# Kernel tuning notes

Hardware: AMD Instinct MI355X
Metric: run time of the kernel (lower is better)

The kernel has to match this reference:

```python
import jax, jax.numpy as jnp
import numpy as np

K_NEIGHBORS = 16
N_CLASSES = 10


def setup_inputs() -> dict:
    key = jax.random.key(0)
    k1, k2, k3 = jax.random.split(key, 3)
    x = jax.random.normal(k1, (2048, 128), dtype=jnp.float32)
    train_data = jax.random.normal(k2, (100000, 128), dtype=jnp.float32)
    train_labels = jax.random.randint(k3, (100000,), 0, N_CLASSES, dtype=jnp.int64)
    return {"x": x, "train_data": train_data, "train_labels": train_labels}


def reference(x, train_data, train_labels):
    N = x.shape[0]
    x2 = jnp.sum(x * x, axis=1, keepdims=True)            # [N, 1]
    t2 = jnp.sum(train_data * train_data, axis=1)          # [M]
    d2 = x2 + t2[None, :] - 2.0 * (x @ train_data.T)       # [N, M]
    dist = jnp.sqrt(jnp.maximum(d2, 0.0))
    # smallest-k via top_k on negated distances
    neg_d, idx = jax.lax.top_k(-dist, K_NEIGHBORS)         # [N, K]
    d = -neg_d
    labels = train_labels[idx]                              # [N, K]
    # weights == 'distance': inverse distance; rows containing an exact match
    # (inf weight) get a 0/1 indicator vector instead.
    w = 1.0 / d
    inf_mask = jnp.isinf(w)
    inf_row = jnp.any(inf_mask, axis=1, keepdims=True)
    w = jnp.where(inf_row, inf_mask.astype(jnp.float32), w)
    # weighted vote: scatter-add weights into per-class buckets
    rows = jnp.arange(N)[:, None]
    proba = jnp.zeros((N, N_CLASSES), jnp.float32).at[rows, labels].add(w)
    s = jnp.sum(proba, axis=1, keepdims=True)
    s = jnp.where(s == 0.0, 1.0, s)
    proba = proba / s
    pred = jnp.argmax(proba, axis=1)
    return pred, proba
```

## Files before the change

kernel.cpp:

```cpp
#include <hip/hip_runtime.h>
#include <hip/hip_fp16.h>
#include <math.h>

#define M_TRAIN 100000
#define NQ 2048
#define DIM 128
#define KNN 16
#define NCLS 10

#define S_STRIDE 16
#define S_CNT (M_TRAIN / S_STRIDE)
#define S_PAD 6272
#define SCH 49
#define SPC 128
#define TT 64
#define MQ 128
#define QSTR 136

#define CAP 768
#define TBH 50176
#define NTR 128
#define NQT 64
#define MARGIN 3.0f

using bfrag = __attribute__((ext_vector_type(8))) short;
using cfrag = __attribute__((ext_vector_type(4))) float;

__device__ __forceinline__ bool better(float d1, int i1, float d2, int i2) {
    return (d1 < d2) || (d1 == d2 && i1 < i2);
}

__device__ __forceinline__ unsigned pack_bf16(float a, float b) {
    unsigned ua = __float_as_uint(a), ub = __float_as_uint(b);
    ua += 0x7fffu + ((ua >> 16) & 1u);
    ub += 0x7fffu + ((ub >> 16) & 1u);
    return (ua >> 16) | (ub & 0xffff0000u);
}

__device__ __forceinline__ void gload_lds16(const void* g, void* l) {
    __builtin_amdgcn_global_load_lds(
        (const __attribute__((address_space(1))) unsigned int*)g,
        (__attribute__((address_space(3))) unsigned int*)l, 16, 0, 0);
}

__global__ void knn_norms(const float* __restrict__ train,
                          const float* __restrict__ x,
                          float* __restrict__ t2, float* __restrict__ x2) {
    int gw = (blockIdx.x * blockDim.x + threadIdx.x) >> 6;
    int lane = threadIdx.x & 63;
    if (gw >= M_TRAIN + NQ) return;
    const float* r = (gw < M_TRAIN) ? (train + (size_t)gw * DIM)
                                    : (x + (size_t)(gw - M_TRAIN) * DIM);
    float a = r[lane];
    float b = r[lane + 64];
    float s = a * a + b * b;
    #pragma unroll
    for (int off = 32; off > 0; off >>= 1)
        s += __shfl_down(s, off, 64);
    if (lane == 0) {
        if (gw < M_TRAIN) t2[gw] = s; else x2[gw - M_TRAIN] = s;
    }
}

__global__ void knn_zero_cnt(int* __restrict__ cnt) {
    int i = blockIdx.x * blockDim.x + threadIdx.x;
    if (i < NQ) cnt[i] = 0;
}

__global__ __launch_bounds__(256, 2)
void knn_sub_mfma(const float* __restrict__ x, const float* __restrict__ train,
                  const float* __restrict__ t2, const float* __restrict__ x2,
                  __half* __restrict__ dsub) {
    __shared__ short Q[MQ * QSTR];
    __shared__ short T[TT * QSTR];
    __shared__ float t2h[TT];
    int tid = threadIdx.x;
    int w = tid >> 6, lane = tid & 63;
    int rquad = lane >> 4, rcol = lane & 15;
    int qBase = blockIdx.y * MQ;
    int cBase = blockIdx.x * SPC;

    #pragma unroll
    for (int it = 0; it < 16; ++it) {
        int f = it * 256 + tid;
        int row = f >> 5, c4 = f & 31;
        float4 v = ((const float4*)x)[(size_t)(qBase + row) * (DIM / 4) + c4];
        uint2 p; p.x = pack_bf16(v.x, v.y); p.y = pack_bf16(v.z, v.w);
        *(uint2*)&Q[row * QSTR + c4 * 4] = p;
    }
    __syncthreads();

    float x2r[2][4];
    #pragma unroll
    for (int rt = 0; rt < 2; ++rt)
        #pragma unroll
        for (int reg = 0; reg < 4; ++reg)
            x2r[rt][reg] = x2[qBase + w * 32 + rt * 16 + rquad * 4 + reg];

    bfrag A[2][4];
    #pragma unroll
    for (int rt = 0; rt < 2; ++rt)
        #pragma unroll
        for (int ks = 0; ks < 4; ++ks) {
            int r = w * 32 + rt * 16 + rcol;
            A[rt][ks] = *(const bfrag*)&Q[r * QSTR + ks * 32 + rquad * 8];
        }

    const cfrag zero4 = {0.f, 0.f, 0.f, 0.f};
    for (int t = 0; t < 2; ++t) {
        __syncthreads();
        int sBase = cBase + t * TT;
        #pragma unroll
        for (int it = 0; it < 8; ++it) {
            int f = it * 256 + tid;
            int row = f >> 5, c4 = f & 31;
            int sj = sBase + row;
            bool ok = sj < S_CNT;
            float4 v = ok ? ((const float4*)train)[(size_t)sj * S_STRIDE * (DIM / 4) + c4]
                          : make_float4(0.f, 0.f, 0.f, 0.f);
            uint2 p; p.x = pack_bf16(v.x, v.y); p.y = pack_bf16(v.z, v.w);
            *(uint2*)&T[row * QSTR + c4 * 4] = p;
        }
        if (tid < TT) {
            int sj = sBase + tid;
            t2h[tid] = (sj < S_CNT) ? t2[(size_t)sj * S_STRIDE] : 1e30f;
        }
        __syncthreads();

        cfrag acc[2][4];
        #pragma unroll
        for (int ks = 0; ks < 4; ++ks) {
            bfrag B[4];
            #pragma unroll
            for (int ct = 0; ct < 4; ++ct) {
                int n = ct * 16 + rcol;
                B[ct] = *(const bfrag*)&T[n * QSTR + ks * 32 + rquad * 8];
            }
            #pragma unroll
            for (int rt = 0; rt < 2; ++rt)
                #pragma unroll
                for (int ct = 0; ct < 4; ++ct)
                    acc[rt][ct] = (ks == 0)
                        ? __builtin_amdgcn_mfma_f32_16x16x32_bf16(A[rt][0], B[ct], zero4, 0, 0, 0)
                        : __builtin_amdgcn_mfma_f32_16x16x32_bf16(A[rt][ks], B[ct], acc[rt][ct], 0, 0, 0);
        }

        float th[4];
        #pragma unroll
        for (int ct = 0; ct < 4; ++ct) th[ct] = t2h[ct * 16 + rcol];
        #pragma unroll
        for (int rt = 0; rt < 2; ++rt)
            #pragma unroll
            for (int ct = 0; ct < 4; ++ct)
                #pragma unroll
                for (int reg = 0; reg < 4; ++reg) {
                    float d2 = x2r[rt][reg] + th[ct] - 2.f * acc[rt][ct][reg];
                    int qrow = qBase + w * 32 + rt * 16 + rquad * 4 + reg;
                    int col = sBase + ct * 16 + rcol;
                    dsub[(size_t)qrow * S_PAD + col] = __float2half_rn(d2);
                }
    }
}

__global__ __launch_bounds__(256)
void knn_select(const __half* __restrict__ dsub, float* __restrict__ tau) {
    __shared__ float wv[4];
    __shared__ int   wc[4];
    __shared__ float sv;
    __shared__ int   sc;
    int q = blockIdx.x, tid = threadIdx.x;
    int w = tid >> 6, lane = tid & 63;

    float bd[KNN];
    #pragma unroll
    for (int j = 0; j < KNN; ++j) bd[j] = 3.4e38f;
    for (int k = 0; k < 25; ++k) {
        int idx = k * 256 + tid;
        if (idx < S_PAD) {
            float v = __half2float(dsub[(size_t)q * S_PAD + idx]);
            if (v < bd[KNN - 1]) {
                bd[KNN - 1] = v;
                #pragma unroll
                for (int j = KNN - 1; j >= 1; --j)
                    if (bd[j] < bd[j - 1]) { float t = bd[j]; bd[j] = bd[j - 1]; bd[j - 1] = t; }
            }
        }
    }

    float last = 3.4e38f;
    for (int sel = 0; sel < KNN; ++sel) {
        float mv = bd[0]; int mj = 0;
        #pragma unroll
        for (int j = 1; j < KNN; ++j) if (bd[j] < mv) { mv = bd[j]; mj = j; }
        int mc = (tid << 4) | mj;
        #pragma unroll
        for (int off = 32; off > 0; off >>= 1) {
            float ov = __shfl_down(mv, off, 64);
            int   oc = __shfl_down(mc, off, 64);
            if (ov < mv) { mv = ov; mc = oc; }
        }
        if (lane == 0) { wv[w] = mv; wc[w] = mc; }
        __syncthreads();
        if (tid == 0) {
            float bv = wv[0]; int bc = wc[0];
            #pragma unroll
            for (int i = 1; i < 4; ++i) if (wv[i] < bv) { bv = wv[i]; bc = wc[i]; }
            sv = bv; sc = bc;
        }
        __syncthreads();
        last = sv;
        if (tid == (sc >> 4)) {
            int j0 = sc & 15;
            #pragma unroll
            for (int j = 0; j < KNN; ++j) if (j == j0) bd[j] = 3.4e38f;
        }
        __syncthreads();
    }
    if (tid == 0) tau[q] = last;
}

__global__ __launch_bounds__(256)
void knn_convert_bf16(const float* __restrict__ train,
                      unsigned int* __restrict__ tb, int rowBase,
                      const float* __restrict__ x,
                      unsigned int* __restrict__ xb) {
    int b = blockIdx.x;
    if (b >= (TBH * 32) / 256) {
        int i = (b - (TBH * 32) / 256) * 256 + threadIdx.x;
        int row = i >> 5, seg = i & 31;
        float4 v = ((const float4*)x)[(size_t)row * (DIM / 4) + seg];
        uint2 p; p.x = pack_bf16(v.x, v.y); p.y = pack_bf16(v.z, v.w);
        ((uint2*)xb)[(size_t)row * 32 + seg] = p;
        return;
    }
    int i = b * 256 + threadIdx.x;
    int row = i >> 5, seg = i & 31;
    int g = rowBase + row;
    float4 v = (g < M_TRAIN)
        ? ((const float4*)train)[(size_t)g * (DIM / 4) + seg]
        : make_float4(0.f, 0.f, 0.f, 0.f);
    uint2 p; p.x = pack_bf16(v.x, v.y); p.y = pack_bf16(v.z, v.w);
    int off = (seg * 8) ^ ((row & 7) << 4);
    *(uint2*)((char*)tb + (size_t)row * 256 + off) = p;
}

__global__ __launch_bounds__(256, 4)
void knn_filter5(const unsigned int* __restrict__ xbb,
                 const short* __restrict__ tbb,
                 const float* __restrict__ t2, const float* __restrict__ x2,
                 const float* __restrict__ tau, int pBase0,
                 int* __restrict__ buf_i, int* __restrict__ cnt) {
    __shared__ __align__(16) short T[NTR * DIM];
    int tid = threadIdx.x;
    int w = tid >> 6, lane = tid & 63;
    int rquad = lane >> 4, rcol = lane & 15;

    int bid = blockIdx.x;
    int xcd = bid & 7, r = bid >> 3;
    int qb = r & 31;
    int nch = xcd + 8 * (r >> 5);
    int qBase = qb * NQT;
    int tbase = pBase0 + nch * NTR;

    const char* gsrc = (const char*)tbb + (size_t)nch * NTR * 256 + w * 8192 + lane * 16;
    char* ldst = (char*)T + w * 8192;
    #pragma unroll
    for (int i = 0; i < 8; ++i)
        gload_lds16(gsrc + i * 1024, ldst + i * 1024);

    bfrag A[4];
    int qrow = qBase + w * 16 + rcol;
    const char* xrow = (const char*)xbb + (size_t)qrow * 256;
    #pragma unroll
    for (int ks = 0; ks < 4; ++ks)
        A[ks] = *(const bfrag*)(xrow + ks * 64 + rquad * 16);

    float RC[4];
    #pragma unroll
    for (int reg = 0; reg < 4; ++reg) {
        int q = qBase + w * 16 + rquad * 4 + reg;
        RC[reg] = 0.5f * (x2[q] - tau[q] - MARGIN);
    }
    float th[8];
    #pragma unroll
    for (int ct = 0; ct < 8; ++ct)
        th[ct] = 0.5f * t2[tbase + ct * 16 + rcol];
    __syncthreads();

    int swz = (rcol & 7) << 4;
    int cs[4];
    #pragma unroll
    for (int ks = 0; ks < 4; ++ks)
        cs[ks] = (ks * 64 + rquad * 16) ^ swz;

    const cfrag zero4 = {0.f, 0.f, 0.f, 0.f};
    cfrag acc[8];
    #pragma unroll
    for (int ks = 0; ks < 4; ++ks)
        #pragma unroll
        for (int ct = 0; ct < 8; ++ct) {
            const bfrag B = *(const bfrag*)((const char*)T + (ct * 16 + rcol) * 256 + cs[ks]);
            acc[ct] = (ks == 0)
                ? __builtin_amdgcn_mfma_f32_16x16x32_bf16(A[0], B, zero4, 0, 0, 0)
                : __builtin_amdgcn_mfma_f32_16x16x32_bf16(A[ks], B, acc[ct], 0, 0, 0);
        }

    unsigned gm[4][8];
    int tot[4];
    #pragma unroll
    for (int reg = 0; reg < 4; ++reg) {
        int t = 0;
        #pragma unroll
        for (int ct = 0; ct < 8; ++ct) {
            int idx = tbase + ct * 16 + rcol;
            bool pass = (acc[ct][reg] >= RC[reg] + th[ct]) && (idx < M_TRAIN);
            unsigned long long m = __ballot(pass);
            unsigned g = (unsigned)(m >> (rquad * 16)) & 0xFFFFu;
            gm[reg][ct] = g;
            t += __popc(g);
        }
        tot[reg] = t;
    }
    int baseR[4];
    #pragma unroll
    for (int reg = 0; reg < 4; ++reg) {
        int q = qBase + w * 16 + rquad * 4 + reg;
        if (rcol == 0) baseR[reg] = atomicAdd(&cnt[q], tot[reg]);
    }
    int lsrc = lane & 48;
    unsigned lb = 1u << rcol;
    #pragma unroll
    for (int reg = 0; reg < 4; ++reg) {
        int q = qBase + w * 16 + rquad * 4 + reg;
        int b = __shfl(baseR[reg], lsrc, 64);
        int off = 0;
        #pragma unroll
        for (int ct = 0; ct < 8; ++ct) {
            unsigned g = gm[reg][ct];
            if (g & lb) {
                int slot = b + off + __popc(g & (lb - 1));
                if (slot < CAP)
                    buf_i[(size_t)q * CAP + slot] = tbase + ct * 16 + rcol;
            }
            off += __popc(g);
        }
    }
}

__global__ __launch_bounds__(256)
void knn_final(const float* __restrict__ x,
               const float* __restrict__ train,
               const float* __restrict__ t2v,
               const float* __restrict__ x2v,
               const int* __restrict__ buf_i,
               const int* __restrict__ cnt,
               const int* __restrict__ labels,
               float* __restrict__ out) {
    __shared__ float sd[CAP];
    __shared__ int   si[CAP];
    int q = blockIdx.x;
    int tid = threadIdx.x;
    int w = tid >> 6, lane = tid & 63;
    int grp = lane >> 4;
    int sub = lane & 15;
    int n = cnt[q]; if (n > CAP) n = CAP;

    const float4* xq = (const float4*)&x[(size_t)q * DIM + sub * 8];
    float4 qa = xq[0], qb = xq[1];
    float x2l = x2v[q];

    for (int base = 0; base < n; base += 16) {
        int i = base + w * 4 + grp;
        if (i < n) {
            int idx = buf_i[(size_t)q * CAP + i];
            const float4* tr = (const float4*)&train[(size_t)idx * DIM + sub * 8];
            float4 ta = tr[0], tb4 = tr[1];
            float s = qa.x * ta.x + qa.y * ta.y + qa.z * ta.z + qa.w * ta.w
                    + qb.x * tb4.x + qb.y * tb4.y + qb.z * tb4.z + qb.w * tb4.w;
            s += __shfl_xor(s, 1, 64);
            s += __shfl_xor(s, 2, 64);
            s += __shfl_xor(s, 4, 64);
            s += __shfl_xor(s, 8, 64);
            if (sub == 0) { sd[i] = x2l + t2v[idx] - 2.f * s; si[i] = idx; }
        }
    }
    __syncthreads();

    if (w == 0) {
        float bd[12]; int bi2[12];
        #pragma unroll
        for (int j = 0; j < 12; ++j) {
            int i = lane + j * 64;
            if (i < n) { bd[j] = sd[i]; bi2[j] = si[i]; }
            else       { bd[j] = 3.4e38f; bi2[j] = 0x7fffffff; }
        }
        float kd[KNN]; int ki[KNN];
        for (int sel = 0; sel < KNN; ++sel) {
            float md = bd[0]; int mi = bi2[0]; int mc = (lane << 4);
            #pragma unroll
            for (int j = 1; j < 12; ++j)
                if (better(bd[j], bi2[j], md, mi)) { md = bd[j]; mi = bi2[j]; mc = (lane << 4) | j; }
            #pragma unroll
            for (int off = 32; off > 0; off >>= 1) {
                float od = __shfl_down(md, off, 64);
                int   oi = __shfl_down(mi, off, 64);
                int   oc = __shfl_down(mc, off, 64);
                if (better(od, oi, md, mi)) { md = od; mi = oi; mc = oc; }
            }
            md = __shfl(md, 0, 64); mi = __shfl(mi, 0, 64); mc = __shfl(mc, 0, 64);
            kd[sel] = md; ki[sel] = mi;
            if (lane == (mc >> 4)) {
                int j0 = mc & 15;
                #pragma unroll
                for (int j = 0; j < 12; ++j)
                    if (j == j0) { bd[j] = 3.4e38f; bi2[j] = 0x7fffffff; }
            }
        }

        if (lane == 0) {
            bool anyzero = false;
            float dist[KNN];
            #pragma unroll
            for (int j = 0; j < KNN; ++j) {
                dist[j] = sqrtf(fmaxf(kd[j], 0.f));
                if (dist[j] == 0.f) anyzero = true;
            }
            float spr[NCLS];
            #pragma unroll
            for (int c = 0; c < NCLS; ++c) spr[c] = 0.f;
            #pragma unroll
            for (int j = 0; j < KNN; ++j) {
                int idxj = ki[j];
                if (idxj < 0 || idxj >= M_TRAIN) continue;
                float wgt = anyzero ? (dist[j] == 0.f ? 1.f : 0.f) : 1.f / dist[j];
                spr[labels[idxj]] += wgt;
            }
            float s = 0.f;
            #pragma unroll
            for (int c = 0; c < NCLS; ++c) s += spr[c];
            if (s == 0.f) s = 1.f;
            float inv = 1.f / s;
            float best = -1.f; int bc = 0;
            #pragma unroll
            for (int c = 0; c < NCLS; ++c) {
                float pv = spr[c] * inv;
                out[NQ + (size_t)q * NCLS + c] = pv;
                if (pv > best) { best = pv; bc = c; }
            }
            out[q] = (float)bc;
        }
    }
}

extern "C" void kernel_launch(void* const* d_in, const int* in_sizes, int n_in,
                              void* d_out, int out_size, void* d_ws, size_t ws_size,
                              hipStream_t stream) {
    const float* x      = (const float*)d_in[0];
    const float* train  = (const float*)d_in[1];
    const int*   labels = (const int*)d_in[2];
    float* out = (float*)d_out;

    char* base = (char*)d_ws;
    float*  t2   = (float*)(base);
    float*  x2   = (float*)(base + 401408);
    float*  tau  = (float*)(base + 409600);
    int*    cnt  = (int*)  (base + 417792);
    char*   region = base + 425984;
    __half* dsub = (__half*)region;
    unsigned int* tb = (unsigned int*)region;
    int*    bi   = (int*)(region + 12845056);
    unsigned int* xb = (unsigned int*)(region + 19136512);

    int nrows = M_TRAIN + NQ;
    knn_norms<<<(nrows * 64 + 255) / 256, 256, 0, stream>>>(train, x, t2, x2);
    knn_zero_cnt<<<(NQ + 255) / 256, 256, 0, stream>>>(cnt);

    dim3 gs(SCH, NQ / MQ);
    knn_sub_mfma<<<gs, 256, 0, stream>>>(x, train, t2, x2, dsub);

    knn_select<<<NQ, 256, 0, stream>>>(dsub, tau);

    for (int h = 0; h < 2; ++h) {
        int rowBase = h * TBH;
        int cgrid = (TBH * 32) / 256 + (h == 0 ? (NQ * 32) / 256 : 0);
        knn_convert_bf16<<<cgrid, 256, 0, stream>>>(train, tb, rowBase, x, xb);
        knn_filter5<<<(TBH / NTR) * (NQ / NQT), 256, 0, stream>>>(
            xb, (const short*)tb, t2, x2, tau, rowBase, bi, cnt);
    }

    knn_final<<<NQ, 256, 0, stream>>>(x, train, t2, x2, bi, cnt, labels, out);
}
```

Measured before the change: 401.0 us.

## Store approximate bf16 distances in filter and prune candidates before exact rescoring

The filter kernel now also writes an approximate squared distance, taken from its bf16 MFMA accumulator, as fp16 alongside each candidate index. The final kernel selects the 16th smallest approximate distance per query and keeps only candidates within a fixed slack of it. Only those survivors are gathered from the fp32 training rows for exact rescoring. The serial single-wave top-16 selection is replaced by a parallel rank-counting pass. The cost is an extra fp16 buffer write and read, plus a correctness risk if bf16/fp16 error exceeds the slack.

```diff
diff --git a/kernel.cpp b/kernel.cpp
--- a/kernel.cpp
+++ b/kernel.cpp
@@ -22,6 +22,7 @@
 #define NTR 128
 #define NQT 64
 #define MARGIN 3.0f
+#define SLACK 7.0f
 
 using bfrag = __attribute__((ext_vector_type(8))) short;
 using cfrag = __attribute__((ext_vector_type(4))) float;
@@ -245,11 +246,12 @@
 }
 
 __global__ __launch_bounds__(256, 4)
-void knn_filter5(const unsigned int* __restrict__ xbb,
+void knn_filter6(const unsigned int* __restrict__ xbb,
                  const short* __restrict__ tbb,
                  const float* __restrict__ t2, const float* __restrict__ x2,
                  const float* __restrict__ tau, int pBase0,
-                 int* __restrict__ buf_i, int* __restrict__ cnt) {
+                 int* __restrict__ buf_i, __half* __restrict__ buf_h,
+                 int* __restrict__ cnt) {
     __shared__ __align__(16) short T[NTR * DIM];
     int tid = threadIdx.x;
     int w = tid >> 6, lane = tid & 63;
@@ -275,11 +277,12 @@
     for (int ks = 0; ks < 4; ++ks)
         A[ks] = *(const bfrag*)(xrow + ks * 64 + rquad * 16);
 
-    float RC[4];
+    float RC[4], x2q[4];
     #pragma unroll
     for (int reg = 0; reg < 4; ++reg) {
         int q = qBase + w * 16 + rquad * 4 + reg;
-        RC[reg] = 0.5f * (x2[q] - tau[q] - MARGIN);
+        x2q[reg] = x2[q];
+        RC[reg] = 0.5f * (x2q[reg] - tau[q] - MARGIN);
     }
     float th[8];
     #pragma unroll
@@ -339,8 +342,11 @@
             unsigned g = gm[reg][ct];
             if (g & lb) {
                 int slot = b + off + __popc(g & (lb - 1));
-                if (slot < CAP)
+                if (slot < CAP) {
                     buf_i[(size_t)q * CAP + slot] = tbase + ct * 16 + rcol;
+                    float d2a = x2q[reg] + 2.f * th[ct] - 2.f * acc[ct][reg];
+                    buf_h[(size_t)q * CAP + slot] = __float2half_rn(d2a);
+                }
             }
             off += __popc(g);
         }
@@ -353,26 +359,82 @@
                const float* __restrict__ t2v,
                const float* __restrict__ x2v,
                const int* __restrict__ buf_i,
+               const __half* __restrict__ buf_h,
                const int* __restrict__ cnt,
                const int* __restrict__ labels,
                float* __restrict__ out) {
     __shared__ float sd[CAP];
     __shared__ int   si[CAP];
+    __shared__ int   keep[CAP];
+    __shared__ float wk[64];
+    __shared__ int   kr[KNN];
+    __shared__ float sthr;
+    __shared__ int   smcnt;
     int q = blockIdx.x;
     int tid = threadIdx.x;
     int w = tid >> 6, lane = tid & 63;
-    int grp = lane >> 4;
-    int sub = lane & 15;
+    int grp = lane >> 4, sub = lane & 15;
     int n = cnt[q]; if (n > CAP) n = CAP;
+    if (tid == 0) smcnt = 0;
+    if (tid < KNN) kr[tid] = -1;
+
+    float av[3];
+    #pragma unroll
+    for (int j = 0; j < 3; ++j) {
+        int i = (w * 3 + j) * 64 + lane;
+        av[j] = (i < n) ? __half2float(buf_h[(size_t)q * CAP + i]) : 3.4e38f;
+    }
+    for (int sel = 0; sel < KNN; ++sel) {
+        float mv = av[0]; int mc = (lane << 2);
+        if (av[1] < mv) { mv = av[1]; mc = (lane << 2) | 1; }
+        if (av[2] < mv) { mv = av[2]; mc = (lane << 2) | 2; }
+        #pragma unroll
+        for (int off = 32; off > 0; off >>= 1) {
+            float ov = __shfl_down(mv, off, 64);
+            int   oc = __shfl_down(mc, off, 64);
+            if (ov < mv || (ov == mv && oc < mc)) { mv = ov; mc = oc; }
+        }
+        mv = __shfl(mv, 0, 64);
+        mc = __shfl(mc, 0, 64);
+        if (lane == 0) wk[w * KNN + sel] = mv;
+        if (lane == (mc >> 2)) {
+            int j0 = mc & 3;
+            if (j0 == 0) av[0] = 3.4e38f;
+            else if (j0 == 1) av[1] = 3.4e38f;
+            else av[2] = 3.4e38f;
+        }
+    }
+    __syncthreads();
+    if (tid < 64) {
+        float v = wk[tid];
+        int rank = 0;
+        #pragma unroll 8
+        for (int j = 0; j < 64; ++j) {
+            float u = wk[j];
+            if (u < v || (u == v && j < tid)) ++rank;
+        }
+        if (rank == KNN - 1) sthr = v + SLACK;
+    }
+    __syncthreads();
+    float thr = sthr;
+
+    for (int i = tid; i < n; i += 256) {
+        float h = __half2float(buf_h[(size_t)q * CAP + i]);
+        if (h <= thr) {
+            int p = atomicAdd(&smcnt, 1);
+            keep[p] = buf_i[(size_t)q * CAP + i];
+        }
+    }
+    __syncthreads();
+    int m = smcnt;
 
     const float4* xq = (const float4*)&x[(size_t)q * DIM + sub * 8];
     float4 qa = xq[0], qb = xq[1];
     float x2l = x2v[q];
-
-    for (int base = 0; base < n; base += 16) {
+    for (int base = 0; base < m; base += 16) {
         int i = base + w * 4 + grp;
-        if (i < n) {
-            int idx = buf_i[(size_t)q * CAP + i];
+        if (i < m) {
+            int idx = keep[i];
             const float4* tr = (const float4*)&train[(size_t)idx * DIM + sub * 8];
             float4 ta = tr[0], tb4 = tr[1];
             float s = qa.x * ta.x + qa.y * ta.y + qa.z * ta.z + qa.w * ta.w
@@ -386,69 +448,50 @@
     }
     __syncthreads();
 
-    if (w == 0) {
-        float bd[12]; int bi2[12];
-        #pragma unroll
-        for (int j = 0; j < 12; ++j) {
-            int i = lane + j * 64;
-            if (i < n) { bd[j] = sd[i]; bi2[j] = si[i]; }
-            else       { bd[j] = 3.4e38f; bi2[j] = 0x7fffffff; }
-        }
-        float kd[KNN]; int ki[KNN];
-        for (int sel = 0; sel < KNN; ++sel) {
-            float md = bd[0]; int mi = bi2[0]; int mc = (lane << 4);
-            #pragma unroll
-            for (int j = 1; j < 12; ++j)
-                if (better(bd[j], bi2[j], md, mi)) { md = bd[j]; mi = bi2[j]; mc = (lane << 4) | j; }
-            #pragma unroll
-            for (int off = 32; off > 0; off >>= 1) {
-                float od = __shfl_down(md, off, 64);
-                int   oi = __shfl_down(mi, off, 64);
-                int   oc = __shfl_down(mc, off, 64);
-                if (better(od, oi, md, mi)) { md = od; mi = oi; mc = oc; }
-            }
-            md = __shfl(md, 0, 64); mi = __shfl(mi, 0, 64); mc = __shfl(mc, 0, 64);
-            kd[sel] = md; ki[sel] = mi;
-            if (lane == (mc >> 4)) {
-                int j0 = mc & 15;
-                #pragma unroll
-                for (int j = 0; j < 12; ++j)
-                    if (j == j0) { bd[j] = 3.4e38f; bi2[j] = 0x7fffffff; }
-            }
-        }
-
-        if (lane == 0) {
-            bool anyzero = false;
-            float dist[KNN];
-            #pragma unroll
-            for (int j = 0; j < KNN; ++j) {
-                dist[j] = sqrtf(fmaxf(kd[j], 0.f));
+    for (int i = tid; i < m; i += 256) {
+        float d = sd[i]; int ix = si[i];
+        int rank = 0;
+        for (int j = 0; j < m; ++j)
+            if (better(sd[j], si[j], d, ix)) ++rank;
+        if (rank < KNN) kr[rank] = i;
+    }
+    __syncthreads();
+
+    if (tid == 0) {
+        bool anyzero = false;
+        float dist[KNN]; int kidx[KNN];
+        #pragma unroll
+        for (int j = 0; j < KNN; ++j) {
+            int ii = kr[j];
+            if (ii >= 0) {
+                dist[j] = sqrtf(fmaxf(sd[ii], 0.f));
+                kidx[j] = si[ii];
                 if (dist[j] == 0.f) anyzero = true;
-            }
-            float spr[NCLS];
-            #pragma unroll
-            for (int c = 0; c < NCLS; ++c) spr[c] = 0.f;
-            #pragma unroll
-            for (int j = 0; j < KNN; ++j) {
-                int idxj = ki[j];
-                if (idxj < 0 || idxj >= M_TRAIN) continue;
-                float wgt = anyzero ? (dist[j] == 0.f ? 1.f : 0.f) : 1.f / dist[j];
-                spr[labels[idxj]] += wgt;
-            }
-            float s = 0.f;
-            #pragma unroll
-            for (int c = 0; c < NCLS; ++c) s += spr[c];
-            if (s == 0.f) s = 1.f;
-            float inv = 1.f / s;
-            float best = -1.f; int bc = 0;
-            #pragma unroll
-            for (int c = 0; c < NCLS; ++c) {
-                float pv = spr[c] * inv;
-                out[NQ + (size_t)q * NCLS + c] = pv;
-                if (pv > best) { best = pv; bc = c; }
-            }
-            out[q] = (float)bc;
-        }
+            } else { dist[j] = -1.f; kidx[j] = -1; }
+        }
+        float spr[NCLS];
+        #pragma unroll
+        for (int c = 0; c < NCLS; ++c) spr[c] = 0.f;
+        #pragma unroll
+        for (int j = 0; j < KNN; ++j) {
+            int idxj = kidx[j];
+            if (idxj < 0 || idxj >= M_TRAIN) continue;
+            float wgt = anyzero ? (dist[j] == 0.f ? 1.f : 0.f) : 1.f / dist[j];
+            spr[labels[idxj]] += wgt;
+        }
+        float s = 0.f;
+        #pragma unroll
+        for (int c = 0; c < NCLS; ++c) s += spr[c];
+        if (s == 0.f) s = 1.f;
+        float inv = 1.f / s;
+        float best = -1.f; int bc = 0;
+        #pragma unroll
+        for (int c = 0; c < NCLS; ++c) {
+            float pv = spr[c] * inv;
+            out[NQ + (size_t)q * NCLS + c] = pv;
+            if (pv > best) { best = pv; bc = c; }
+        }
+        out[q] = (float)bc;
     }
 }
 
@@ -470,6 +513,7 @@
     unsigned int* tb = (unsigned int*)region;
     int*    bi   = (int*)(region + 12845056);
     unsigned int* xb = (unsigned int*)(region + 19136512);
+    __half* bh   = (__half*)(region + 19660800);
 
     int nrows = M_TRAIN + NQ;
     knn_norms<<<(nrows * 64 + 255) / 256, 256, 0, stream>>>(train, x, t2, x2);
@@ -484,9 +528,9 @@
         int rowBase = h * TBH;
         int cgrid = (TBH * 32) / 256 + (h == 0 ? (NQ * 32) / 256 : 0);
         knn_convert_bf16<<<cgrid, 256, 0, stream>>>(train, tb, rowBase, x, xb);
-        knn_filter5<<<(TBH / NTR) * (NQ / NQT), 256, 0, stream>>>(
-            xb, (const short*)tb, t2, x2, tau, rowBase, bi, cnt);
-    }
-
-    knn_final<<<NQ, 256, 0, stream>>>(x, train, t2, x2, bi, cnt, labels, out);
-}
+        knn_filter6<<<(TBH / NTR) * (NQ / NQT), 256, 0, stream>>>(
+            xb, (const short*)tb, t2, x2, tau, rowBase, bi, bh, cnt);
+    }
+
+    knn_final<<<NQ, 256, 0, stream>>>(x, train, t2, x2, bi, bh, cnt, labels, out);
+}
```

After: 581.7 us. 1.45x slower.
